# Kernel tuning notes

Hardware: AMD Instinct MI355X
Metric: run time of the kernel (lower is better)

Reference implementation:

```python
import jax, jax.numpy as jnp
import numpy as np

N_NODES = 50000
N_EDGES = 800000
D = 512
N_LAYERS = 3
LN_EPS = 1e-5


def _layer_norm(h, gamma, beta):
    mu = jnp.mean(h, axis=-1, keepdims=True)
    var = jnp.mean(jnp.square(h - mu), axis=-1, keepdims=True)
    return (h - mu) * jax.lax.rsqrt(var + LN_EPS) * gamma + beta


def setup_inputs() -> dict:
    key = jax.random.key(0)
    ks = jax.random.split(key, 5)
    x = jax.random.normal(ks[0], (N_NODES, D), dtype=jnp.float32)
    edge_index = jax.random.randint(ks[1], (2, N_EDGES), 0, N_NODES, dtype=jnp.int64)
    edge_weight = jax.random.uniform(ks[2], (N_EDGES,), dtype=jnp.float32)
    # GCNConv lin weights (xavier-ish scale), zero biases; LayerNorm affine params
    Ws = jax.random.normal(ks[3], (N_LAYERS, D, D), dtype=jnp.float32) * (1.0 / np.sqrt(D))
    bs = jnp.zeros((N_LAYERS, D), dtype=jnp.float32)
    gammas = jnp.ones((N_LAYERS, D), dtype=jnp.float32)
    betas = jnp.zeros((N_LAYERS, D), dtype=jnp.float32)
    return {"x": x, "edge_index": edge_index, "edge_weight": edge_weight,
            "Ws": Ws, "bs": bs, "gammas": gammas, "betas": betas}


def reference(x, edge_index, edge_weight, Ws, bs, gammas, betas):
    n = x.shape[0]
    row, col = edge_index[0], edge_index[1]  # source -> target (PyG convention)
    # add self loops with weight 1 (GCNConv add_self_loops=True)
    sl = jnp.arange(n, dtype=edge_index.dtype)
    row2 = jnp.concatenate([row, sl])
    col2 = jnp.concatenate([col, sl])
    ew = jnp.concatenate([edge_weight, jnp.ones((n,), dtype=edge_weight.dtype)])
    # symmetric normalization: D^{-1/2} A D^{-1/2}
    deg = jax.ops.segment_sum(ew, col2, num_segments=n)
    dinv = jnp.where(deg > 0, 1.0 / jnp.sqrt(jnp.where(deg > 0, deg, 1.0)), 0.0)
    norm = dinv[row2] * ew * dinv[col2]  # [E+N]

    for i in range(N_LAYERS):
        identity = x
        h = x @ Ws[i].T                       # [N, D] linear transform
        msg = norm[:, None] * h[row2]         # gather + scale per edge
        agg = jax.ops.segment_sum(msg, col2, num_segments=n) + bs[i]
        h = _layer_norm(agg, gammas[i], betas[i])
        if i < N_LAYERS - 1:
            h = jax.nn.relu(h)                # dropout=0 -> identity
        x = h + identity                      # residual (dims equal -> Identity proj)
    return x
```

## Files before the change

kernel.cpp:

```cpp
#include <hip/hip_runtime.h>
#include <hip/hip_bf16.h>
#include <stdint.h>

#define D 512
#define LN_EPS 1e-5f

typedef __attribute__((ext_vector_type(8))) short bf16x8;
typedef __attribute__((ext_vector_type(4))) float f32x4;

__device__ __forceinline__ unsigned short f32_to_bf16_bits(float x) {
    unsigned int u = __float_as_uint(x);
    u += 0x7fffu + ((u >> 16) & 1u);
    return (unsigned short)(u >> 16);
}
__device__ __forceinline__ float bf16lo(unsigned int u) { return __uint_as_float(u << 16); }
__device__ __forceinline__ float bf16hi(unsigned int u) { return __uint_as_float(u & 0xffff0000u); }

typedef const __attribute__((address_space(1))) unsigned int GU;
typedef __attribute__((address_space(3))) unsigned int LU;
__device__ __forceinline__ void gload_lds16(const void* g, void* l) {
    __builtin_amdgcn_global_load_lds((GU*)g, (LU*)l, 16, 0, 0);
}

__global__ void k_prep(const float4* __restrict__ x0, ushort4* __restrict__ xb4,
                       const float4* __restrict__ Ws4, ushort4* __restrict__ wb4,
                       float* __restrict__ deg, int* __restrict__ cnt,
                       long nx4, long nxin4, long nw4, int N) {
    long id = (long)blockIdx.x * blockDim.x + threadIdx.x;
    if (id < nx4) {
        float4 v;
        if (id < nxin4) v = x0[id];
        else { v.x = 0.f; v.y = 0.f; v.z = 0.f; v.w = 0.f; }
        ushort4 o;
        o.x = f32_to_bf16_bits(v.x);
        o.y = f32_to_bf16_bits(v.y);
        o.z = f32_to_bf16_bits(v.z);
        o.w = f32_to_bf16_bits(v.w);
        xb4[id] = o;
    } else if (id < nx4 + nw4) {
        long i = id - nx4;
        float4 v = Ws4[i];
        ushort4 o;
        o.x = f32_to_bf16_bits(v.x);
        o.y = f32_to_bf16_bits(v.y);
        o.z = f32_to_bf16_bits(v.z);
        o.w = f32_to_bf16_bits(v.w);
        wb4[i] = o;
    } else {
        long i = id - nx4 - nw4;
        if (i < N) { deg[i] = 1.0f; cnt[i] = 1; }
    }
}

__global__ void k_deg_cnt(const int* __restrict__ col, const float* __restrict__ ew,
                          float* deg, int* cnt, int E) {
    int e = blockIdx.x * blockDim.x + threadIdx.x;
    if (e < E) {
        int c = col[e];
        atomicAdd(&deg[c], ew[e]);
        atomicAdd(&cnt[c], 1);
    }
}

__global__ __launch_bounds__(1024) void k_scan(const int* __restrict__ cnt,
                                               int* __restrict__ rptr,
                                               int* __restrict__ cur, int n) {
    const int tid = threadIdx.x, lane = tid & 63, wv = tid >> 6;
    const int chunk = (n + 15) >> 4;
    const int wbeg = wv * chunk;
    const int wend = min(wbeg + chunk, n);

    int tot = 0;
    for (int i = wbeg + lane; i < wend; i += 64) tot += cnt[i];
#pragma unroll
    for (int off = 32; off > 0; off >>= 1) tot += __shfl_xor(tot, off);
    __shared__ int woff[17];
    if (lane == 0) woff[wv] = tot;
    __syncthreads();
    if (tid == 0) {
        int r = 0;
        for (int w = 0; w < 16; ++w) { int t = woff[w]; woff[w] = r; r += t; }
        woff[16] = r;
    }
    __syncthreads();

    int run = woff[wv];
    for (int base = wbeg; base < wend; base += 64) {
        int i = base + lane;
        int v = (i < wend) ? cnt[i] : 0;
        int inc = v;
#pragma unroll
        for (int off = 1; off < 64; off <<= 1) {
            int u = __shfl_up(inc, off);
            if (lane >= off) inc += u;
        }
        if (i < wend) {
            int excl = run + inc - v;
            rptr[i] = excl;
            cur[i] = excl;
        }
        run += __shfl(inc, 63);
    }
    if (tid == 0) rptr[n] = woff[16];
}

__global__ void k_fill(const int* __restrict__ row, const int* __restrict__ col,
                       const float* __restrict__ ew, const float* __restrict__ deg,
                       int* cur, uint2* __restrict__ srcval, int N, int E) {
    int i = blockIdx.x * blockDim.x + threadIdx.x;
    if (i < N) {
        int slot = atomicAdd(&cur[i], 1);
        uint2 sv; sv.x = (unsigned)i; sv.y = __float_as_uint(1.0f / deg[i]);
        srcval[slot] = sv;
    } else if (i < N + E) {
        int e = i - N;
        int r = row[e], c = col[e];
        int slot = atomicAdd(&cur[c], 1);
        uint2 sv; sv.x = (unsigned)r;
        sv.y = __float_as_uint(rsqrtf(deg[r]) * ew[e] * rsqrtf(deg[c]));
        srcval[slot] = sv;
    }
}

__global__ __launch_bounds__(512) void k_gemm(
    const short* __restrict__ A,
    const short* __restrict__ W,
    short* __restrict__ H,
    int Mpad) {
    __shared__ short As[3][128 * 32];
    __shared__ short Bs[3][256 * 32];
    const int tid = threadIdx.x;
    const int wave = tid >> 6, lane = tid & 63;
    const int wm = (wave >> 2) * 64, wn = (wave & 3) * 64;
    const int tm = blockIdx.x * 128, tn = blockIdx.y * 256;
    f32x4 acc[4][4] = {};
    const int fr = lane & 15, fc = lane >> 4;

    const int r0 = tid >> 2, cb0 = (tid & 3) * 8;
    const short* Ab = A + (size_t)(tm + r0) * 512 + cb0;
    const short* Wb = W + (size_t)(tn + r0) * 512 + cb0;

#define STAGE(t)                                                            \
    {                                                                       \
        const int _k = (t) * 32, _b = (t) % 3;                              \
        gload_lds16(Ab + _k,                     &As[_b][tid * 8]);         \
        gload_lds16(Wb + _k,                     &Bs[_b][tid * 8]);         \
        gload_lds16(Wb + (size_t)128 * 512 + _k, &Bs[_b][(tid + 512) * 8]); \
    }

    STAGE(0);
    STAGE(1);
#pragma unroll
    for (int t = 0; t < 16; ++t) {
        if (t < 15) asm volatile("s_waitcnt vmcnt(3)" ::: "memory");
        else        asm volatile("s_waitcnt vmcnt(0)" ::: "memory");
        __builtin_amdgcn_s_barrier();
        asm volatile("" ::: "memory");
        if (t < 14) STAGE(t + 2);
        const int b = t % 3;
        bf16x8 af[4], bfr[4];
#pragma unroll
        for (int m = 0; m < 4; ++m)
            af[m] = *(const bf16x8*)&As[b][(wm + m * 16 + fr) * 32 + fc * 8];
#pragma unroll
        for (int n = 0; n < 4; ++n)
            bfr[n] = *(const bf16x8*)&Bs[b][(wn + n * 16 + fr) * 32 + fc * 8];
#pragma unroll
        for (int m = 0; m < 4; ++m) {
#pragma unroll
            for (int n = 0; n < 4; ++n)
                acc[m][n] = __builtin_amdgcn_mfma_f32_16x16x32_bf16(af[m], bfr[n], acc[m][n], 0, 0, 0);
        }
    }
#undef STAGE
    const int cbase = tn + wn + (lane & 15);
    const int rbase = tm + wm + fc * 4;
#pragma unroll
    for (int m = 0; m < 4; ++m) {
#pragma unroll
        for (int n = 0; n < 4; ++n) {
#pragma unroll
            for (int j = 0; j < 4; ++j) {
                int r = rbase + m * 16 + j;
                int c = cbase + n * 16;
                H[(size_t)r * 512 + c] = (short)f32_to_bf16_bits(acc[m][n][j]);
            }
        }
    }
}

__global__ __launch_bounds__(256) void k_agg_ln(
    const uint4* __restrict__ H4,
    const int* __restrict__ rptr,
    const uint2* __restrict__ srcval,
    const float4* __restrict__ bias,
    const float4* __restrict__ gamma,
    const float4* __restrict__ beta,
    uint4* __restrict__ xb,
    float4* __restrict__ out_f32,
    int N, int last) {
    const int wv = threadIdx.x >> 6, lane = threadIdx.x & 63;
    const int t = blockIdx.x * 4 + wv;
    if (t >= N) return;
    const int beg = rptr[t], end = rptr[t + 1];

    float a[8], b[8];
#pragma unroll
    for (int i = 0; i < 8; ++i) { a[i] = 0.f; b[i] = 0.f; }

    for (int base = beg; base < end; base += 64) {
        int m = end - base;
        if (m > 64) m = 64;
        int idx = base + lane;
        if (idx > end - 1) idx = end - 1;
        uint2 svl = srcval[idx];
        int e = 0;
        for (; e + 2 <= m; e += 2) {
            unsigned s0 = __shfl(svl.x, e);
            unsigned s1 = __shfl(svl.x, e + 1);
            float w0 = __uint_as_float(__shfl(svl.y, e));
            float w1 = __uint_as_float(__shfl(svl.y, e + 1));
            uint4 u0 = H4[(size_t)s0 * 64 + lane];
            uint4 u1 = H4[(size_t)s1 * 64 + lane];
            a[0] = fmaf(w0, bf16lo(u0.x), a[0]);
            a[1] = fmaf(w0, bf16hi(u0.x), a[1]);
            a[2] = fmaf(w0, bf16lo(u0.y), a[2]);
            a[3] = fmaf(w0, bf16hi(u0.y), a[3]);
            a[4] = fmaf(w0, bf16lo(u0.z), a[4]);
            a[5] = fmaf(w0, bf16hi(u0.z), a[5]);
            a[6] = fmaf(w0, bf16lo(u0.w), a[6]);
            a[7] = fmaf(w0, bf16hi(u0.w), a[7]);
            b[0] = fmaf(w1, bf16lo(u1.x), b[0]);
            b[1] = fmaf(w1, bf16hi(u1.x), b[1]);
            b[2] = fmaf(w1, bf16lo(u1.y), b[2]);
            b[3] = fmaf(w1, bf16hi(u1.y), b[3]);
            b[4] = fmaf(w1, bf16lo(u1.z), b[4]);
            b[5] = fmaf(w1, bf16hi(u1.z), b[5]);
            b[6] = fmaf(w1, bf16lo(u1.w), b[6]);
            b[7] = fmaf(w1, bf16hi(u1.w), b[7]);
        }
        if (e < m) {
            unsigned s0 = __shfl(svl.x, e);
            float w0 = __uint_as_float(__shfl(svl.y, e));
            uint4 u0 = H4[(size_t)s0 * 64 + lane];
            a[0] = fmaf(w0, bf16lo(u0.x), a[0]);
            a[1] = fmaf(w0, bf16hi(u0.x), a[1]);
            a[2] = fmaf(w0, bf16lo(u0.y), a[2]);
            a[3] = fmaf(w0, bf16hi(u0.y), a[3]);
            a[4] = fmaf(w0, bf16lo(u0.z), a[4]);
            a[5] = fmaf(w0, bf16hi(u0.z), a[5]);
            a[6] = fmaf(w0, bf16lo(u0.w), a[6]);
            a[7] = fmaf(w0, bf16hi(u0.w), a[7]);
        }
    }
#pragma unroll
    for (int i = 0; i < 8; ++i) a[i] += b[i];

    float4 bv0 = bias[lane * 2], bv1 = bias[lane * 2 + 1];
    a[0] += bv0.x; a[1] += bv0.y; a[2] += bv0.z; a[3] += bv0.w;
    a[4] += bv1.x; a[5] += bv1.y; a[6] += bv1.z; a[7] += bv1.w;

    float s1 = 0.f, s2 = 0.f;
#pragma unroll
    for (int i = 0; i < 8; ++i) { s1 += a[i]; s2 += a[i] * a[i]; }
#pragma unroll
    for (int off = 32; off > 0; off >>= 1) {
        s1 += __shfl_xor(s1, off);
        s2 += __shfl_xor(s2, off);
    }
    const float mean = s1 * (1.0f / 512.0f);
    const float var = s2 * (1.0f / 512.0f) - mean * mean;
    const float rstd = rsqrtf(var + LN_EPS);

    float4 gv0 = gamma[lane * 2], gv1 = gamma[lane * 2 + 1];
    float4 bt0 = beta[lane * 2], bt1 = beta[lane * 2 + 1];
    float o[8];
    o[0] = (a[0] - mean) * rstd * gv0.x + bt0.x;
    o[1] = (a[1] - mean) * rstd * gv0.y + bt0.y;
    o[2] = (a[2] - mean) * rstd * gv0.z + bt0.z;
    o[3] = (a[3] - mean) * rstd * gv0.w + bt0.w;
    o[4] = (a[4] - mean) * rstd * gv1.x + bt1.x;
    o[5] = (a[5] - mean) * rstd * gv1.y + bt1.y;
    o[6] = (a[6] - mean) * rstd * gv1.z + bt1.z;
    o[7] = (a[7] - mean) * rstd * gv1.w + bt1.w;
    if (!last) {
#pragma unroll
        for (int i = 0; i < 8; ++i) o[i] = fmaxf(o[i], 0.f);
    }
    uint4 idu = xb[(size_t)t * 64 + lane];
    o[0] += bf16lo(idu.x); o[1] += bf16hi(idu.x);
    o[2] += bf16lo(idu.y); o[3] += bf16hi(idu.y);
    o[4] += bf16lo(idu.z); o[5] += bf16hi(idu.z);
    o[6] += bf16lo(idu.w); o[7] += bf16hi(idu.w);

    if (last) {
        float4 f0, f1;
        f0.x = o[0]; f0.y = o[1]; f0.z = o[2]; f0.w = o[3];
        f1.x = o[4]; f1.y = o[5]; f1.z = o[6]; f1.w = o[7];
        out_f32[(size_t)t * 128 + lane * 2] = f0;
        out_f32[(size_t)t * 128 + lane * 2 + 1] = f1;
    } else {
        uint4 pk;
        pk.x = ((unsigned)f32_to_bf16_bits(o[1]) << 16) | f32_to_bf16_bits(o[0]);
        pk.y = ((unsigned)f32_to_bf16_bits(o[3]) << 16) | f32_to_bf16_bits(o[2]);
        pk.z = ((unsigned)f32_to_bf16_bits(o[5]) << 16) | f32_to_bf16_bits(o[4]);
        pk.w = ((unsigned)f32_to_bf16_bits(o[7]) << 16) | f32_to_bf16_bits(o[6]);
        xb[(size_t)t * 64 + lane] = pk;
    }
}

extern "C" void kernel_launch(void* const* d_in, const int* in_sizes, int n_in,
                              void* d_out, int out_size, void* d_ws, size_t ws_size,
                              hipStream_t stream) {
    const float* x0     = (const float*)d_in[0];
    const int*   ei     = (const int*)d_in[1];
    const float* ew     = (const float*)d_in[2];
    const float* Ws     = (const float*)d_in[3];
    const float* bs     = (const float*)d_in[4];
    const float* gammas = (const float*)d_in[5];
    const float* betas  = (const float*)d_in[6];

    const int N = in_sizes[0] / D;
    const int E = in_sizes[1] / 2;
    const int L = in_sizes[3] / (D * D);
    const int Mpad = (N + 127) & ~127;

    char* p = (char*)d_ws;
    auto carve = [&](size_t bytes) {
        char* q = p;
        p += (bytes + 255) & ~(size_t)255;
        return (void*)q;
    };
    short* xb     = (short*)carve((size_t)Mpad * D * 2);
    short* hb     = (short*)carve((size_t)Mpad * D * 2);
    short* wb     = (short*)carve((size_t)L * D * D * 2);
    float* deg    = (float*)carve((size_t)N * 4);
    int*   cnt    = (int*)carve((size_t)N * 4);
    int*   rptr   = (int*)carve((size_t)(N + 1) * 4);
    int*   cur    = (int*)carve((size_t)N * 4);
    uint2* srcval = (uint2*)carve((size_t)(E + N) * 8);
    (void)ws_size; (void)n_in; (void)out_size;

    const int* rowI = ei;
    const int* colI = ei + E;

    {
        long nx4 = (long)Mpad * D / 4, nxin4 = (long)N * D / 4;
        long nw4 = (long)L * D * D / 4;
        long tot = nx4 + nw4 + N;
        k_prep<<<(int)((tot + 255) / 256), 256, 0, stream>>>(
            (const float4*)x0, (ushort4*)xb, (const float4*)Ws, (ushort4*)wb,
            deg, cnt, nx4, nxin4, nw4, N);
    }
    k_deg_cnt<<<(E + 255) / 256, 256, 0, stream>>>(colI, ew, deg, cnt, E);
    k_scan<<<1, 1024, 0, stream>>>(cnt, rptr, cur, N);
    k_fill<<<(N + E + 255) / 256, 256, 0, stream>>>(rowI, colI, ew, deg, cur, srcval, N, E);

    for (int l = 0; l < L; ++l) {
        dim3 g(Mpad / 128, D / 256);
        k_gemm<<<g, 512, 0, stream>>>(xb, wb + (size_t)l * D * D, hb, Mpad);
        int last = (l == L - 1);
        k_agg_ln<<<(N + 3) / 4, 256, 0, stream>>>(
            (const uint4*)hb, rptr, srcval,
            (const float4*)(bs + (size_t)l * D),
            (const float4*)(gammas + (size_t)l * D),
            (const float4*)(betas + (size_t)l * D),
            (uint4*)xb, (float4*)d_out, N, last);
    }
}
```

Before: 685.2 us.

## Pack degree and count into one double atomic; stage GEMM epilogue through LDS

The degree sum and in-edge count are packed into a single double (count in the high part, scaled by 2^32), so each edge needs one 64-bit float atomic instead of two 32-bit atomics. The GEMM epilogue now writes bf16 results into a padded per-wave LDS tile and then emits coalesced 16-byte row stores, replacing scattered 2-byte stores to H. The packed double gives up some low-order precision on the degree value and depends on hardware double atomics. The LDS reuse adds a barrier after the main loop.

```diff
diff --git a/kernel.cpp b/kernel.cpp
--- a/kernel.cpp
+++ b/kernel.cpp
@@ -4,6 +4,7 @@
 
 #define D 512
 #define LN_EPS 1e-5f
+#define TWO32 4294967296.0
 
 typedef __attribute__((ext_vector_type(8))) short bf16x8;
 typedef __attribute__((ext_vector_type(4))) float f32x4;
@@ -16,6 +17,14 @@
 __device__ __forceinline__ float bf16lo(unsigned int u) { return __uint_as_float(u << 16); }
 __device__ __forceinline__ float bf16hi(unsigned int u) { return __uint_as_float(u & 0xffff0000u); }
 
+__device__ __forceinline__ float unpack_deg(double d) {
+    int c = (int)(d * (1.0 / TWO32));
+    return (float)(d - TWO32 * (double)c);
+}
+__device__ __forceinline__ int unpack_cnt(double d) {
+    return (int)(d * (1.0 / TWO32));
+}
+
 typedef const __attribute__((address_space(1))) unsigned int GU;
 typedef __attribute__((address_space(3))) unsigned int LU;
 __device__ __forceinline__ void gload_lds16(const void* g, void* l) {
@@ -24,7 +33,7 @@
 
 __global__ void k_prep(const float4* __restrict__ x0, ushort4* __restrict__ xb4,
                        const float4* __restrict__ Ws4, ushort4* __restrict__ wb4,
-                       float* __restrict__ deg, int* __restrict__ cnt,
+                       double* __restrict__ dp,
                        long nx4, long nxin4, long nw4, int N) {
     long id = (long)blockIdx.x * blockDim.x + threadIdx.x;
     if (id < nx4) {
@@ -48,21 +57,17 @@
         wb4[i] = o;
     } else {
         long i = id - nx4 - nw4;
-        if (i < N) { deg[i] = 1.0f; cnt[i] = 1; }
+        if (i < N) dp[i] = TWO32 + 1.0;
     }
 }
 
 __global__ void k_deg_cnt(const int* __restrict__ col, const float* __restrict__ ew,
-                          float* deg, int* cnt, int E) {
+                          double* dp, int E) {
     int e = blockIdx.x * blockDim.x + threadIdx.x;
-    if (e < E) {
-        int c = col[e];
-        atomicAdd(&deg[c], ew[e]);
-        atomicAdd(&cnt[c], 1);
-    }
-}
-
-__global__ __launch_bounds__(1024) void k_scan(const int* __restrict__ cnt,
+    if (e < E) atomicAdd(&dp[col[e]], TWO32 + (double)ew[e]);
+}
+
+__global__ __launch_bounds__(1024) void k_scan(const double* __restrict__ dp,
                                                int* __restrict__ rptr,
                                                int* __restrict__ cur, int n) {
     const int tid = threadIdx.x, lane = tid & 63, wv = tid >> 6;
@@ -71,7 +76,7 @@
     const int wend = min(wbeg + chunk, n);
 
     int tot = 0;
-    for (int i = wbeg + lane; i < wend; i += 64) tot += cnt[i];
+    for (int i = wbeg + lane; i < wend; i += 64) tot += unpack_cnt(dp[i]);
 #pragma unroll
     for (int off = 32; off > 0; off >>= 1) tot += __shfl_xor(tot, off);
     __shared__ int woff[17];
@@ -87,7 +92,7 @@
     int run = woff[wv];
     for (int base = wbeg; base < wend; base += 64) {
         int i = base + lane;
-        int v = (i < wend) ? cnt[i] : 0;
+        int v = (i < wend) ? unpack_cnt(dp[i]) : 0;
         int inc = v;
 #pragma unroll
         for (int off = 1; off < 64; off <<= 1) {
@@ -105,19 +110,20 @@
 }
 
 __global__ void k_fill(const int* __restrict__ row, const int* __restrict__ col,
-                       const float* __restrict__ ew, const float* __restrict__ deg,
+                       const float* __restrict__ ew, const double* __restrict__ dp,
                        int* cur, uint2* __restrict__ srcval, int N, int E) {
     int i = blockIdx.x * blockDim.x + threadIdx.x;
     if (i < N) {
         int slot = atomicAdd(&cur[i], 1);
-        uint2 sv; sv.x = (unsigned)i; sv.y = __float_as_uint(1.0f / deg[i]);
+        uint2 sv; sv.x = (unsigned)i;
+        sv.y = __float_as_uint(1.0f / unpack_deg(dp[i]));
         srcval[slot] = sv;
     } else if (i < N + E) {
         int e = i - N;
         int r = row[e], c = col[e];
         int slot = atomicAdd(&cur[c], 1);
         uint2 sv; sv.x = (unsigned)r;
-        sv.y = __float_as_uint(rsqrtf(deg[r]) * ew[e] * rsqrtf(deg[c]));
+        sv.y = __float_as_uint(rsqrtf(unpack_deg(dp[r])) * ew[e] * rsqrtf(unpack_deg(dp[c])));
         srcval[slot] = sv;
     }
 }
@@ -127,8 +133,9 @@
     const short* __restrict__ W,
     short* __restrict__ H,
     int Mpad) {
-    __shared__ short As[3][128 * 32];
-    __shared__ short Bs[3][256 * 32];
+    __shared__ short smem[3 * 128 * 32 + 3 * 256 * 32];
+    short (*As)[128 * 32] = (short(*)[128 * 32])smem;
+    short (*Bs)[256 * 32] = (short(*)[256 * 32])(smem + 3 * 128 * 32);
     const int tid = threadIdx.x;
     const int wave = tid >> 6, lane = tid & 63;
     const int wm = (wave >> 2) * 64, wn = (wave & 3) * 64;
@@ -173,19 +180,29 @@
         }
     }
 #undef STAGE
-    const int cbase = tn + wn + (lane & 15);
-    const int rbase = tm + wm + fc * 4;
+
+    __syncthreads();
+
+    short* wlds = smem + wave * (64 * 72);
 #pragma unroll
     for (int m = 0; m < 4; ++m) {
 #pragma unroll
         for (int n = 0; n < 4; ++n) {
 #pragma unroll
-            for (int j = 0; j < 4; ++j) {
-                int r = rbase + m * 16 + j;
-                int c = cbase + n * 16;
-                H[(size_t)r * 512 + c] = (short)f32_to_bf16_bits(acc[m][n][j]);
-            }
-        }
+            for (int j = 0; j < 4; ++j)
+                wlds[(m * 16 + fc * 4 + j) * 72 + n * 16 + fr] =
+                    (short)f32_to_bf16_bits(acc[m][n][j]);
+        }
+    }
+    asm volatile("s_waitcnt lgkmcnt(0)" ::: "memory");
+    __builtin_amdgcn_sched_barrier(0);
+
+    const int ch = lane & 7, rg = lane >> 3;
+#pragma unroll
+    for (int i = 0; i < 8; ++i) {
+        const int rrow = i * 8 + rg;
+        bf16x8 v = *(const bf16x8*)&wlds[rrow * 72 + ch * 8];
+        *(bf16x8*)&H[(size_t)(tm + wm + rrow) * 512 + tn + wn + ch * 8] = v;
     }
 }
 
@@ -331,14 +348,13 @@
         p += (bytes + 255) & ~(size_t)255;
         return (void*)q;
     };
-    short* xb     = (short*)carve((size_t)Mpad * D * 2);
-    short* hb     = (short*)carve((size_t)Mpad * D * 2);
-    short* wb     = (short*)carve((size_t)L * D * D * 2);
-    float* deg    = (float*)carve((size_t)N * 4);
-    int*   cnt    = (int*)carve((size_t)N * 4);
-    int*   rptr   = (int*)carve((size_t)(N + 1) * 4);
-    int*   cur    = (int*)carve((size_t)N * 4);
-    uint2* srcval = (uint2*)carve((size_t)(E + N) * 8);
+    short*  xb     = (short*)carve((size_t)Mpad * D * 2);
+    short*  hb     = (short*)carve((size_t)Mpad * D * 2);
+    short*  wb     = (short*)carve((size_t)L * D * D * 2);
+    double* dp     = (double*)carve((size_t)N * 8);
+    int*    rptr   = (int*)carve((size_t)(N + 1) * 4);
+    int*    cur    = (int*)carve((size_t)N * 4);
+    uint2*  srcval = (uint2*)carve((size_t)(E + N) * 8);
     (void)ws_size; (void)n_in; (void)out_size;
 
     const int* rowI = ei;
@@ -350,11 +366,11 @@
         long tot = nx4 + nw4 + N;
         k_prep<<<(int)((tot + 255) / 256), 256, 0, stream>>>(
             (const float4*)x0, (ushort4*)xb, (const float4*)Ws, (ushort4*)wb,
-            deg, cnt, nx4, nxin4, nw4, N);
-    }
-    k_deg_cnt<<<(E + 255) / 256, 256, 0, stream>>>(colI, ew, deg, cnt, E);
-    k_scan<<<1, 1024, 0, stream>>>(cnt, rptr, cur, N);
-    k_fill<<<(N + E + 255) / 256, 256, 0, stream>>>(rowI, colI, ew, deg, cur, srcval, N, E);
+            dp, nx4, nxin4, nw4, N);
+    }
+    k_deg_cnt<<<(E + 255) / 256, 256, 0, stream>>>(colI, ew, dp, E);
+    k_scan<<<1, 1024, 0, stream>>>(dp, rptr, cur, N);
+    k_fill<<<(N + E + 255) / 256, 256, 0, stream>>>(rowI, colI, ew, dp, cur, srcval, N, E);
 
     for (int l = 0; l < L; ++l) {
         dim3 g(Mpad / 128, D / 256);
```

Measured after the change: 656.5 us (median of 2 runs). 1.04x faster.
